# Kernel optimization log

Hardware: AMD Instinct MI355X
Metric: run time of the kernel (lower is better)

The kernel has to match this reference:

```python
import jax, jax.numpy as jnp
import numpy as np

N_NODES = 100000
N_EDGES = 1600000
IN_FEATS = 128
HEADS = 8
OUT_FEATS = 16
NEG_SLOPE = 0.2


def setup_inputs() -> dict:
    key = jax.random.key(0)
    ks = jax.random.split(key, 7)
    feats = jax.random.normal(ks[0], (N_NODES, IN_FEATS), dtype=jnp.float32)
    W = jax.random.normal(ks[1], (IN_FEATS, HEADS * OUT_FEATS), dtype=jnp.float32) * (1.0 / np.sqrt(IN_FEATS))
    attn_l = jax.random.normal(ks[2], (HEADS, OUT_FEATS), dtype=jnp.float32) * 0.1
    attn_r = jax.random.normal(ks[3], (HEADS, OUT_FEATS), dtype=jnp.float32) * 0.1
    bias_vec = jax.random.normal(ks[4], (HEADS * OUT_FEATS,), dtype=jnp.float32) * 0.01
    src = jax.random.randint(ks[5], (N_EDGES,), 0, N_NODES, dtype=jnp.int32)
    dst = jax.random.randint(ks[6], (N_EDGES,), 0, N_NODES, dtype=jnp.int32)
    return {"feats": feats, "W": W, "attn_l": attn_l, "attn_r": attn_r,
            "bias_vec": bias_vec, "src": src, "dst": dst}


def reference(feats, W, attn_l, attn_r, bias_vec, src, dst):
    N = feats.shape[0]
    H, D = attn_l.shape
    # linear projection (feat_drop = 0 in eval): [N, H, D]
    h = (feats @ W).reshape(N, H, D)
    # per-node attention halves: [N, H]
    el = jnp.einsum('nhd,hd->nh', h, attn_l)
    er = jnp.einsum('nhd,hd->nh', h, attn_r)
    # per-edge score with LeakyReLU: [E, H]
    e = jax.nn.leaky_relu(el[src] + er[dst], negative_slope=NEG_SLOPE)
    # edge softmax segmented by destination node
    seg_max = jax.ops.segment_max(e, dst, num_segments=N)            # [N, H]
    seg_max = jnp.where(jnp.isfinite(seg_max), seg_max, 0.0)          # zero-in-degree guard
    exp_e = jnp.exp(e - seg_max[dst])                                 # [E, H]
    seg_sum = jax.ops.segment_sum(exp_e, dst, num_segments=N)        # [N, H]
    alpha = exp_e / seg_sum[dst]                                      # [E, H]
    # weighted gather-scatter aggregation: [N, H, D]
    msg = alpha[:, :, None] * h[src]
    rst = jax.ops.segment_sum(msg, dst, num_segments=N)
    # identity residual (in_feats == H*D) + bias, then flatten
    rst = rst + h + bias_vec.reshape(1, H, D)
    return rst.reshape(N, H * D)
```

## Files before the change

kernel.cpp:

```cpp
#include <hip/hip_runtime.h>

#define NEG 0.2f
#define CHUNK 2048
#define BINW 48

using bf16x8 = __attribute__((ext_vector_type(8))) short;
using f32x4  = __attribute__((ext_vector_type(4))) float;
using f32x2  = __attribute__((ext_vector_type(2))) float;

__device__ __forceinline__ short f2bf(float f) {
    union { float f; unsigned u; } v; v.f = f;
    unsigned r = v.u + 0x7FFFu + ((v.u >> 16) & 1u);
    return (short)(r >> 16);
}
__device__ __forceinline__ float bflo(unsigned v) {
    union { unsigned u; float f; } x; x.u = v << 16; return x.f;
}
__device__ __forceinline__ float bfhi(unsigned v) {
    union { unsigned u; float f; } x; x.u = v & 0xffff0000u; return x.f;
}

__global__ __launch_bounds__(256) void k_wt(const float* __restrict__ W,
                                            unsigned short* __restrict__ Wbf) {
    int idx = (blockIdx.x * 256 + threadIdx.x) * 4;
    #pragma unroll
    for (int q = 0; q < 4; ++q) {
        int i = idx + q;
        int k = i >> 7, c = i & 127;
        Wbf[c * 128 + k] = (unsigned short)f2bf(W[i]);
    }
}

__global__ __launch_bounds__(256) void k_fill(const int* __restrict__ src,
                                              const int* __restrict__ dst,
                                              int* __restrict__ cnt,
                                              int* __restrict__ bins,
                                              int E, int N8) {
    int b = blockIdx.x;
    int r = b & 7;
    int c = b >> 3;
    int lo = r * N8, hi = lo + N8;
    int base = c * CHUNK + threadIdx.x;
    #pragma unroll
    for (int q = 0; q < 8; ++q) {
        int e = base + q * 256;
        if (e < E) {
            int d = dst[e];
            if (d >= lo && d < hi) {
                int p = atomicAdd(&cnt[d], 1);
                if (p < BINW) bins[(size_t)d * BINW + p] = src[e];
            }
        }
    }
}

__global__ __launch_bounds__(256) void k_gemm(const float* __restrict__ feats,
                                              const unsigned short* __restrict__ Wbf,
                                              unsigned short* __restrict__ h,
                                              const float* __restrict__ attn_l,
                                              const float* __restrict__ attn_r,
                                              float* __restrict__ el,
                                              float* __restrict__ er,
                                              unsigned char* __restrict__ h8,
                                              int N) {
    __shared__ __align__(16) short Wt[128 * 136];
    const int t = threadIdx.x;
    const int n0 = blockIdx.x * 64;

    {
        const uint4* Ws = (const uint4*)Wbf;
        #pragma unroll
        for (int i = 0; i < 8; ++i) {
            int g = t * 8 + i;
            int c = g >> 4, j = g & 15;
            *(uint4*)&Wt[c * 136 + j * 8] = Ws[g];
        }
    }
    __syncthreads();

    const int w    = t >> 6;
    const int lane = t & 63;
    const int m    = lane & 15;
    const int quad = lane >> 4;
    const int kq   = quad * 8;

    const int row_a = n0 + w * 16 + m;
    const bool va = (row_a < N);

    f32x4 acc[8];
    #pragma unroll
    for (int ti = 0; ti < 8; ++ti) acc[ti] = (f32x4){0.f, 0.f, 0.f, 0.f};

    #pragma unroll
    for (int kc = 0; kc < 4; ++kc) {
        const float* ap = feats + (size_t)row_a * 128 + kc * 32 + kq;
        float4 a0 = va ? ((const float4*)ap)[0] : make_float4(0.f,0.f,0.f,0.f);
        float4 a1 = va ? ((const float4*)ap)[1] : make_float4(0.f,0.f,0.f,0.f);
        bf16x8 af;
        af[0] = f2bf(a0.x); af[1] = f2bf(a0.y); af[2] = f2bf(a0.z); af[3] = f2bf(a0.w);
        af[4] = f2bf(a1.x); af[5] = f2bf(a1.y); af[6] = f2bf(a1.z); af[7] = f2bf(a1.w);
        #pragma unroll
        for (int ti = 0; ti < 8; ++ti) {
            bf16x8 bf = *(const bf16x8*)&Wt[(ti * 16 + m) * 136 + kc * 32 + kq];
            acc[ti] = __builtin_amdgcn_mfma_f32_16x16x32_bf16(af, bf, acc[ti], 0, 0, 0);
        }
    }

    __syncthreads();
    short* hs = Wt;
    const int row_l = w * 16 + quad * 4;
    #pragma unroll
    for (int ti = 0; ti < 8; ++ti) {
        int col = ti * 16 + m;
        #pragma unroll
        for (int r = 0; r < 4; ++r)
            hs[(row_l + r) * 136 + col] = f2bf(acc[ti][r]);
    }
    __syncthreads();

    #pragma unroll
    for (int u = 0; u < 2; ++u) {
        int p = u * 256 + t;
        int row = p >> 3, hd = p & 7;
        int rg = n0 + row;
        if (rg < N) {
            const uint4* hp = (const uint4*)&hs[row * 136 + hd * 16];
            uint4 u0 = hp[0], u1 = hp[1];

            uint4* hg = (uint4*)(h + (size_t)rg * 128 + hd * 16);
            hg[0] = u0; hg[1] = u1;

            float hv[16];
            hv[0]=bflo(u0.x); hv[1]=bfhi(u0.x); hv[2]=bflo(u0.y); hv[3]=bfhi(u0.y);
            hv[4]=bflo(u0.z); hv[5]=bfhi(u0.z); hv[6]=bflo(u0.w); hv[7]=bfhi(u0.w);
            hv[8]=bflo(u1.x); hv[9]=bfhi(u1.x); hv[10]=bflo(u1.y); hv[11]=bfhi(u1.y);
            hv[12]=bflo(u1.z); hv[13]=bfhi(u1.z); hv[14]=bflo(u1.w); hv[15]=bfhi(u1.w);

            unsigned p0 = 0, p1 = 0, p2 = 0, p3 = 0;
            p0 = __builtin_amdgcn_cvt_pk_fp8_f32(hv[0],  hv[1],  p0, false);
            p0 = __builtin_amdgcn_cvt_pk_fp8_f32(hv[2],  hv[3],  p0, true);
            p1 = __builtin_amdgcn_cvt_pk_fp8_f32(hv[4],  hv[5],  p1, false);
            p1 = __builtin_amdgcn_cvt_pk_fp8_f32(hv[6],  hv[7],  p1, true);
            p2 = __builtin_amdgcn_cvt_pk_fp8_f32(hv[8],  hv[9],  p2, false);
            p2 = __builtin_amdgcn_cvt_pk_fp8_f32(hv[10], hv[11], p2, true);
            p3 = __builtin_amdgcn_cvt_pk_fp8_f32(hv[12], hv[13], p3, false);
            p3 = __builtin_amdgcn_cvt_pk_fp8_f32(hv[14], hv[15], p3, true);
            *(uint4*)(h8 + (size_t)rg * 128 + hd * 16) = make_uint4(p0, p1, p2, p3);

            const float4* al = (const float4*)(attn_l + hd * 16);
            const float4* ar = (const float4*)(attn_r + hd * 16);
            float sl = 0.f, sr = 0.f;
            #pragma unroll
            for (int q = 0; q < 4; ++q) {
                float4 a = al[q], b = ar[q];
                sl += hv[4*q]*a.x + hv[4*q+1]*a.y + hv[4*q+2]*a.z + hv[4*q+3]*a.w;
                sr += hv[4*q]*b.x + hv[4*q+1]*b.y + hv[4*q+2]*b.z + hv[4*q+3]*b.w;
            }
            el[rg * 8 + hd] = sl;
            er[rg * 8 + hd] = sr;
        }
    }
}

__global__ __launch_bounds__(256) void k_agg(const int* __restrict__ cnt,
                                             const int* __restrict__ bins,
                                             const float* __restrict__ el,
                                             const float* __restrict__ er,
                                             const unsigned char* __restrict__ h8,
                                             const unsigned short* __restrict__ h,
                                             const float* __restrict__ bias,
                                             float* __restrict__ out, int N) {
    int nb = gridDim.x;
    int b  = blockIdx.x;
    int g  = ((nb & 7) == 0) ? ((b & 7) * (nb >> 3) + (b >> 3)) : b;

    int t = threadIdx.x;
    int n = g * 4 + (t >> 6);
    if (n >= N) return;
    int lane = t & 63;
    int q    = lane >> 4;
    int c16  = lane & 15;
    int hd   = c16 >> 1;
    int deg  = cnt[n];
    if (deg > BINW) deg = BINW;
    int begin = n * BINW;
    int end   = begin + deg;
    float erv = er[n * 8 + hd];

    float acc[8] = {0.f,0.f,0.f,0.f,0.f,0.f,0.f,0.f};
    float expsum = 0.f;

    auto edge = [&](int p) {
        int s = bins[p];
        float x = el[s * 8 + hd] + erv;
        x = x > 0.f ? x : NEG * x;
        float w = __expf(x);
        expsum += w;
        uint2 hv = *(const uint2*)(h8 + (size_t)s * 128 + c16 * 8);
        f32x2 d0 = __builtin_amdgcn_cvt_pk_f32_fp8(hv.x, false);
        f32x2 d1 = __builtin_amdgcn_cvt_pk_f32_fp8(hv.x, true);
        f32x2 d2 = __builtin_amdgcn_cvt_pk_f32_fp8(hv.y, false);
        f32x2 d3 = __builtin_amdgcn_cvt_pk_f32_fp8(hv.y, true);
        acc[0] += w * d0[0]; acc[1] += w * d0[1];
        acc[2] += w * d1[0]; acc[3] += w * d1[1];
        acc[4] += w * d2[0]; acc[5] += w * d2[1];
        acc[6] += w * d3[0]; acc[7] += w * d3[1];
    };

    int p = begin + q;
    for (; p + 12 < end; p += 16) { edge(p); edge(p + 4); edge(p + 8); edge(p + 12); }
    for (; p < end; p += 4) edge(p);

    #pragma unroll
    for (int k = 0; k < 8; ++k) {
        acc[k] += __shfl_xor(acc[k], 32);
        acc[k] += __shfl_xor(acc[k], 16);
    }
    expsum += __shfl_xor(expsum, 32);
    expsum += __shfl_xor(expsum, 16);

    if (q == 0) {
        float inv = expsum > 0.f ? 1.f / expsum : 0.f;
        uint4 hn = *(const uint4*)(h + (size_t)n * 128 + c16 * 8);
        const float4* bp = (const float4*)(bias + c16 * 8);
        float4 b0 = bp[0], b1 = bp[1];
        float4 o0, o1;
        o0.x = acc[0]*inv + bflo(hn.x) + b0.x;
        o0.y = acc[1]*inv + bfhi(hn.x) + b0.y;
        o0.z = acc[2]*inv + bflo(hn.y) + b0.z;
        o0.w = acc[3]*inv + bfhi(hn.y) + b0.w;
        o1.x = acc[4]*inv + bflo(hn.z) + b1.x;
        o1.y = acc[5]*inv + bfhi(hn.z) + b1.y;
        o1.z = acc[6]*inv + bflo(hn.w) + b1.z;
        o1.w = acc[7]*inv + bfhi(hn.w) + b1.w;
        float4* op = (float4*)(out + (size_t)n * 128 + c16 * 8);
        op[0] = o0; op[1] = o1;
    }
}

extern "C" void kernel_launch(void* const* d_in, const int* in_sizes, int n_in,
                              void* d_out, int out_size, void* d_ws, size_t ws_size,
                              hipStream_t stream) {
    const float* feats  = (const float*)d_in[0];
    const float* W      = (const float*)d_in[1];
    const float* attn_l = (const float*)d_in[2];
    const float* attn_r = (const float*)d_in[3];
    const float* bias   = (const float*)d_in[4];
    const int*   src    = (const int*)d_in[5];
    const int*   dst    = (const int*)d_in[6];

    const int N  = in_sizes[0] / 128;
    const int E  = in_sizes[5];
    const int N8 = (N + 7) / 8;
    const int CH = (E + CHUNK - 1) / CHUNK;
    const int GB = (N + 63) / 64;

    float* out = (float*)d_out;
    char*  ws  = (char*)d_ws;
    unsigned short* Wbf = (unsigned short*)ws;         ws += 128 * 128 * 2;
    unsigned short* h = (unsigned short*)ws;           ws += (size_t)N * 128 * 2;
    unsigned char* h8 = (unsigned char*)ws;            ws += (size_t)N * 128;
    float* el      = (float*)ws;                       ws += (size_t)N * 8 * 4;
    float* er      = (float*)ws;                       ws += (size_t)N * 8 * 4;
    int*   cnt     = (int*)ws;                         ws += (size_t)N * 4;
    int*   bins    = (int*)ws;                         ws += (size_t)N * BINW * 4;

    hipMemsetAsync(cnt, 0, (size_t)N * sizeof(int), stream);

    k_wt   <<<16,          256, 0, stream>>>(W, Wbf);
    k_gemm <<<GB,          256, 0, stream>>>(feats, Wbf, h, attn_l, attn_r, el, er, h8, N);
    k_fill <<<CH * 8,      256, 0, stream>>>(src, dst, cnt, bins, E, N8);
    k_agg  <<<(N + 3) / 4, 256, 0, stream>>>(cnt, bins, el, er, h8, h, bias, out, N);
}
```

Before: 286.1 us.

## Merge edge binning and GEMM into one kernel, fold count reset into transpose

The edge-binning fill and the projection GEMM now run as one launch, with the first blocks doing binning and the rest doing the GEMM, so the two independent phases can share the GPU. The count array is zeroed inside the weight transpose kernel instead of by a separate memset. The 8-way destination-range partitioning of the fill is dropped, so each edge is read once rather than eight times, but atomics now hit random destinations across the whole array. Binning blocks still allocate the GEMM's large shared-memory tile, which can limit how many of them are resident at once.

```diff
diff --git a/kernel.cpp b/kernel.cpp
--- a/kernel.cpp
+++ b/kernel.cpp
@@ -21,7 +21,8 @@
 }
 
 __global__ __launch_bounds__(256) void k_wt(const float* __restrict__ W,
-                                            unsigned short* __restrict__ Wbf) {
+                                            unsigned short* __restrict__ Wbf,
+                                            int* __restrict__ cnt, int N) {
     int idx = (blockIdx.x * 256 + threadIdx.x) * 4;
     #pragma unroll
     for (int q = 0; q < 4; ++q) {
@@ -29,43 +30,42 @@
         int k = i >> 7, c = i & 127;
         Wbf[c * 128 + k] = (unsigned short)f2bf(W[i]);
     }
-}
-
-__global__ __launch_bounds__(256) void k_fill(const int* __restrict__ src,
-                                              const int* __restrict__ dst,
-                                              int* __restrict__ cnt,
-                                              int* __restrict__ bins,
-                                              int E, int N8) {
-    int b = blockIdx.x;
-    int r = b & 7;
-    int c = b >> 3;
-    int lo = r * N8, hi = lo + N8;
-    int base = c * CHUNK + threadIdx.x;
-    #pragma unroll
-    for (int q = 0; q < 8; ++q) {
-        int e = base + q * 256;
-        if (e < E) {
-            int d = dst[e];
-            if (d >= lo && d < hi) {
+    for (int i = blockIdx.x * 256 + threadIdx.x; i < N; i += gridDim.x * 256)
+        cnt[i] = 0;
+}
+
+__global__ __launch_bounds__(256) void k_fg(const float* __restrict__ feats,
+                                            const unsigned short* __restrict__ Wbf,
+                                            unsigned short* __restrict__ h,
+                                            const float* __restrict__ attn_l,
+                                            const float* __restrict__ attn_r,
+                                            float* __restrict__ el,
+                                            float* __restrict__ er,
+                                            unsigned char* __restrict__ h8,
+                                            const int* __restrict__ src,
+                                            const int* __restrict__ dst,
+                                            int* __restrict__ cnt,
+                                            int* __restrict__ bins,
+                                            int N, int E, int FB) {
+    __shared__ __align__(16) short Wt[128 * 136];
+
+    if (blockIdx.x < FB) {
+        int base = blockIdx.x * CHUNK + threadIdx.x;
+        #pragma unroll
+        for (int q = 0; q < 8; ++q) {
+            int e = base + q * 256;
+            if (e < E) {
+                int d = dst[e];
+                int s = src[e];
                 int p = atomicAdd(&cnt[d], 1);
-                if (p < BINW) bins[(size_t)d * BINW + p] = src[e];
+                if (p < BINW) bins[(size_t)d * BINW + p] = s;
             }
         }
-    }
-}
-
-__global__ __launch_bounds__(256) void k_gemm(const float* __restrict__ feats,
-                                              const unsigned short* __restrict__ Wbf,
-                                              unsigned short* __restrict__ h,
-                                              const float* __restrict__ attn_l,
-                                              const float* __restrict__ attn_r,
-                                              float* __restrict__ el,
-                                              float* __restrict__ er,
-                                              unsigned char* __restrict__ h8,
-                                              int N) {
-    __shared__ __align__(16) short Wt[128 * 136];
+        return;
+    }
+
     const int t = threadIdx.x;
-    const int n0 = blockIdx.x * 64;
+    const int n0 = (blockIdx.x - FB) * 64;
 
     {
         const uint4* Ws = (const uint4*)Wbf;
@@ -251,8 +251,7 @@
 
     const int N  = in_sizes[0] / 128;
     const int E  = in_sizes[5];
-    const int N8 = (N + 7) / 8;
-    const int CH = (E + CHUNK - 1) / CHUNK;
+    const int FB = (E + CHUNK - 1) / CHUNK;
     const int GB = (N + 63) / 64;
 
     float* out = (float*)d_out;
@@ -265,10 +264,8 @@
     int*   cnt     = (int*)ws;                         ws += (size_t)N * 4;
     int*   bins    = (int*)ws;                         ws += (size_t)N * BINW * 4;
 
-    hipMemsetAsync(cnt, 0, (size_t)N * sizeof(int), stream);
-
-    k_wt   <<<16,          256, 0, stream>>>(W, Wbf);
-    k_gemm <<<GB,          256, 0, stream>>>(feats, Wbf, h, attn_l, attn_r, el, er, h8, N);
-    k_fill <<<CH * 8,      256, 0, stream>>>(src, dst, cnt, bins, E, N8);
-    k_agg  <<<(N + 3) / 4, 256, 0, stream>>>(cnt, bins, el, er, h8, h, bias, out, N);
-}
+    k_wt <<<16,          256, 0, stream>>>(W, Wbf, cnt, N);
+    k_fg <<<FB + GB,     256, 0, stream>>>(feats, Wbf, h, attn_l, attn_r, el, er, h8,
+                                           src, dst, cnt, bins, N, E, FB);
+    k_agg <<<(N + 3) / 4, 256, 0, stream>>>(cnt, bins, el, er, h8, h, bias, out, N);
+}
```

After: 344.0 us. +20.2%, slower.
